# Kernel optimization log

Measured on AMD Instinct MI355X. Metric: run time of the kernel, lower is better.

Reference implementation:

```python
import jax, jax.numpy as jnp
import numpy as np

WINDOW = 128
CAUSAL = True
LOOK_BACKWARD = 1
LOOK_FORWARD = 0  # causal forces look_forward = 0


def _look_around(x, backward, forward, pad_value, dim):
    # pad along window axis (axis=1), then concat shifted slices along `dim`
    nw = x.shape[1]
    pad_cfg = [(0, 0)] * x.ndim
    pad_cfg[1] = (backward, forward)
    padded = jnp.pad(x, pad_cfg, constant_values=pad_value)
    slices = [padded[:, i:i + nw] for i in range(forward + backward + 1)]
    return jnp.concatenate(slices, axis=dim)


def setup_inputs() -> dict:
    key = jax.random.key(0)
    kq, kk, kv = jax.random.split(key, 3)
    shape = (2, 16, 4096, 64)
    return {
        "q": jax.random.normal(kq, shape, dtype=jnp.float32),
        "k": jax.random.normal(kk, shape, dtype=jnp.float32),
        "v": jax.random.normal(kv, shape, dtype=jnp.float32),
    }


def reference(q, k, v):
    b, h, t, e = q.shape
    scale = e ** (-0.5)
    windows = t // WINDOW  # t assumed divisible by WINDOW (pad_to_multiple is no-op)

    # merge batch and heads, bucket into windows
    bq = q.reshape(b * h, windows, WINDOW, e)
    bk = k.reshape(b * h, windows, WINDOW, e)
    bv = v.reshape(b * h, windows, WINDOW, e)

    # look-around gather of key/value windows: j-dim = WINDOW*(1+back+fwd)
    bk = _look_around(bk, LOOK_BACKWARD, LOOK_FORWARD, 0.0, dim=2)
    bv = _look_around(bv, LOOK_BACKWARD, LOOK_FORWARD, 0.0, dim=2)

    # positional indices for masking
    bq_t = jnp.arange(t).reshape(1, windows, WINDOW)
    bq_k = _look_around(bq_t, LOOK_BACKWARD, LOOK_FORWARD, -1, dim=2)

    mask = (bq_k == -1)[:, :, None, :]  # (1, w, 1, j) padded positions
    if CAUSAL:
        mask = mask | (bq_t[:, :, :, None] < bq_k[:, :, None, :])

    dots = jnp.einsum('bwie,bwje->bwij', bq * scale, bk)
    mask_value = -jnp.finfo(dots.dtype).max
    dots = jnp.where(mask, mask_value, dots)
    attn = jax.nn.softmax(dots.astype(jnp.float32), axis=-1).astype(dots.dtype)
    out = jnp.einsum('bwij,bwje->bwie', attn, bv)
    return out.reshape(b, h, t, e)
```

## Files before the change

### kernel.cpp

```cpp
#include <hip/hip_runtime.h>

#define T_DIM 4096
#define E_DIM 64
#define WIN   128
#define NWIN  (T_DIM / WIN)
#define KS_LD 72
#define VT_LD 136
#define PS_LD 36

typedef __bf16  bf16x8 __attribute__((ext_vector_type(8)));
typedef __bf16  bf16x4 __attribute__((ext_vector_type(4)));
typedef float   f32x16 __attribute__((ext_vector_type(16)));

template<int CTRL>
__device__ __forceinline__ float dppf(float x) {
  return __int_as_float(__builtin_amdgcn_update_dpp(0, __float_as_int(x), CTRL, 0xf, 0xf, false));
}
__device__ __forceinline__ float rsum32(float x) {
  x += dppf<0xB1>(x);
  x += dppf<0x4E>(x);
  x += dppf<0x141>(x);
  x += dppf<0x140>(x);
  x += __int_as_float(__builtin_amdgcn_ds_swizzle(__float_as_int(x), 0x401F));
  return x;
}

__global__ __launch_bounds__(256, 3)
void la_fwd(const float* __restrict__ Q, const float* __restrict__ K,
            const float* __restrict__ V, float* __restrict__ O)
{
  __shared__ __bf16 Ks[WIN * KS_LD];
  __shared__ __bf16 Vt[E_DIM * VT_LD];
  __shared__ __bf16 Psm[4 * 32 * PS_LD];

  const int tid  = threadIdx.x;
  const int lane = tid & 63;
  const int wid  = tid >> 6;
  const int col  = lane & 31;
  const int half = lane >> 5;

  const int w  = blockIdx.x;
  const int bh = blockIdx.y;

  const float* Qb = Q + (size_t)bh * T_DIM * E_DIM;
  const float* Kb = K + (size_t)bh * T_DIM * E_DIM;
  const float* Vb = V + (size_t)bh * T_DIM * E_DIM;
  float*       Ob = O + (size_t)bh * T_DIM * E_DIM;

  const int q0 = w * WIN;

  const float QS = 0.125f * 1.44269504088896340736f;
  bf16x8 aq[4];
  {
    const float* qrow = Qb + (size_t)(q0 + wid * 32 + col) * E_DIM;
#pragma unroll
    for (int c = 0; c < 4; ++c) {
      const float* p = qrow + c * 16 + half * 8;
      const float4 x = *(const float4*)(p);
      const float4 y = *(const float4*)(p + 4);
      bf16x8 a;
      a[0]=(__bf16)(x.x*QS); a[1]=(__bf16)(x.y*QS); a[2]=(__bf16)(x.z*QS); a[3]=(__bf16)(x.w*QS);
      a[4]=(__bf16)(y.x*QS); a[5]=(__bf16)(y.y*QS); a[6]=(__bf16)(y.z*QS); a[7]=(__bf16)(y.w*QS);
      aq[c] = a;
    }
  }

  float lr[16];
  f32x16 oacc[2];
#pragma unroll
  for (int r = 0; r < 16; ++r) lr[r] = 0.0f;
#pragma unroll
  for (int et = 0; et < 2; ++et)
#pragma unroll
    for (int r = 0; r < 16; ++r) oacc[et][r] = 0.0f;

  __bf16* Ps = Psm + wid * (32 * PS_LD);

  auto stage = [&](int kr0) {
    const float* kp = Kb + (size_t)kr0 * E_DIM;
#pragma unroll 4
    for (int i = 0; i < 8; ++i) {
      const int fi = (i << 10) + (tid << 2);
      const float4 kv = *(const float4*)(kp + fi);
      const int row = fi >> 6, cole = fi & 63;
      bf16x4 k4; k4[0]=(__bf16)kv.x; k4[1]=(__bf16)kv.y; k4[2]=(__bf16)kv.z; k4[3]=(__bf16)kv.w;
      *(bf16x4*)(&Ks[row * KS_LD + cole]) = k4;
    }
    const int j  = tid & 127;
    const int ch = (tid >> 7) * 32;
    const float* vrow = Vb + (size_t)(kr0 + j) * E_DIM + ch;
#pragma unroll 4
    for (int c4 = 0; c4 < 8; ++c4) {
      const float4 vv = *(const float4*)(vrow + c4 * 4);
      const int e = ch + c4 * 4;
      Vt[(e + 0) * VT_LD + j] = (__bf16)vv.x;
      Vt[(e + 1) * VT_LD + j] = (__bf16)vv.y;
      Vt[(e + 2) * VT_LD + j] = (__bf16)vv.z;
      Vt[(e + 3) * VT_LD + j] = (__bf16)vv.w;
    }
  };

  auto kb_step = [&](int kb, bool diag) {
    f32x16 s;
#pragma unroll
    for (int r = 0; r < 16; ++r) s[r] = 0.0f;
#pragma unroll
    for (int c = 0; c < 4; ++c) {
      const bf16x8 bk = *(const bf16x8*)(&Ks[(kb * 32 + col) * KS_LD + c * 16 + half * 8]);
      s = __builtin_amdgcn_mfma_f32_32x32x16_bf16(aq[c], bk, s, 0, 0, 0);
    }
#pragma unroll
    for (int r = 0; r < 16; ++r) {
      const int row = (r & 3) + 8 * (r >> 2) + 4 * half;
      float sv = s[r];
      if (diag && col > row) sv = -3.0e38f;
      const float p = __builtin_amdgcn_exp2f(sv);
      lr[r] += p;
      Ps[row * PS_LD + col] = (__bf16)p;
    }
    bf16x8 ap[2];
#pragma unroll
    for (int c2 = 0; c2 < 2; ++c2) {
      const __bf16* rp = Ps + col * PS_LD + c2 * 16 + half * 8;
      union { bf16x8 v8; bf16x4 v4[2]; } u;
      u.v4[0] = *(const bf16x4*)(rp);
      u.v4[1] = *(const bf16x4*)(rp + 4);
      ap[c2] = u.v8;
    }
#pragma unroll
    for (int c2 = 0; c2 < 2; ++c2) {
      const int j0 = kb * 32 + c2 * 16 + half * 8;
#pragma unroll
      for (int et = 0; et < 2; ++et) {
        const bf16x8 bv = *(const bf16x8*)(&Vt[(et * 32 + col) * VT_LD + j0]);
        oacc[et] = __builtin_amdgcn_mfma_f32_32x32x16_bf16(ap[c2], bv, oacc[et], 0, 0, 0);
      }
    }
  };

  if (w > 0) {
    stage(q0 - WIN);
    __syncthreads();
#pragma unroll
    for (int kb = 0; kb < 4; ++kb) kb_step(kb, false);
    __syncthreads();
  }

  stage(q0);
  __syncthreads();
  for (int kb = 0; kb <= wid; ++kb) kb_step(kb, kb == wid);

#pragma unroll
  for (int r = 0; r < 16; ++r) {
    const int row  = (r & 3) + 8 * (r >> 2) + 4 * half;
    const float rinv = __builtin_amdgcn_rcpf(rsum32(lr[r]));
    float* op = Ob + (size_t)(q0 + wid * 32 + row) * E_DIM;
    op[col]      = oacc[0][r] * rinv;
    op[col + 32] = oacc[1][r] * rinv;
  }
}

extern "C" void kernel_launch(void* const* d_in, const int* in_sizes, int n_in,
                              void* d_out, int out_size, void* d_ws, size_t ws_size,
                              hipStream_t stream) {
  const float* Q = (const float*)d_in[0];
  const float* K = (const float*)d_in[1];
  const float* V = (const float*)d_in[2];
  float*       O = (float*)d_out;
  const int bh = in_sizes[0] / (T_DIM * E_DIM);
  dim3 grid(NWIN, bh);
  la_fwd<<<grid, 256, 0, stream>>>(Q, K, V, O);
}
```

Measured before the change: 148.3 us.

## Compute transposed S so P stays in registers; read K directly from global

```diff
diff --git a/kernel.cpp b/kernel.cpp
--- a/kernel.cpp
+++ b/kernel.cpp
@@ -4,34 +4,17 @@
 #define E_DIM 64
 #define WIN   128
 #define NWIN  (T_DIM / WIN)
-#define KS_LD 72
 #define VT_LD 136
-#define PS_LD 36
 
 typedef __bf16  bf16x8 __attribute__((ext_vector_type(8)));
-typedef __bf16  bf16x4 __attribute__((ext_vector_type(4)));
 typedef float   f32x16 __attribute__((ext_vector_type(16)));
 
-template<int CTRL>
-__device__ __forceinline__ float dppf(float x) {
-  return __int_as_float(__builtin_amdgcn_update_dpp(0, __float_as_int(x), CTRL, 0xf, 0xf, false));
-}
-__device__ __forceinline__ float rsum32(float x) {
-  x += dppf<0xB1>(x);
-  x += dppf<0x4E>(x);
-  x += dppf<0x141>(x);
-  x += dppf<0x140>(x);
-  x += __int_as_float(__builtin_amdgcn_ds_swizzle(__float_as_int(x), 0x401F));
-  return x;
-}
-
-__global__ __launch_bounds__(256, 3)
+__global__ __launch_bounds__(256, 4)
 void la_fwd(const float* __restrict__ Q, const float* __restrict__ K,
             const float* __restrict__ V, float* __restrict__ O)
 {
-  __shared__ __bf16 Ks[WIN * KS_LD];
-  __shared__ __bf16 Vt[E_DIM * VT_LD];
-  __shared__ __bf16 Psm[4 * 32 * PS_LD];
+  __shared__ __align__(16) __bf16 Vt0[E_DIM * VT_LD];
+  __shared__ __align__(16) __bf16 Vt1[E_DIM * VT_LD];
 
   const int tid  = threadIdx.x;
   const int lane = tid & 63;
@@ -49,8 +32,25 @@
 
   const int q0 = w * WIN;
 
+  auto stage = [&](int kr0, __bf16* Vt) {
+    const int j  = tid & 127;
+    const int ch = (tid >> 7) * 32;
+    const float* vrow = Vb + (size_t)(kr0 + j) * E_DIM + ch;
+#pragma unroll
+    for (int c4 = 0; c4 < 8; ++c4) {
+      const float4 vv = *(const float4*)(vrow + c4 * 4);
+      const int e = ch + c4 * 4;
+      Vt[(e + 0) * VT_LD + j] = (__bf16)vv.x;
+      Vt[(e + 1) * VT_LD + j] = (__bf16)vv.y;
+      Vt[(e + 2) * VT_LD + j] = (__bf16)vv.z;
+      Vt[(e + 3) * VT_LD + j] = (__bf16)vv.w;
+    }
+  };
+  if (w > 0) stage(q0 - WIN, Vt0);
+  stage(q0, Vt1);
+
   const float QS = 0.125f * 1.44269504088896340736f;
-  bf16x8 aq[4];
+  bf16x8 bq[4];
   {
     const float* qrow = Qb + (size_t)(q0 + wid * 32 + col) * E_DIM;
 #pragma unroll
@@ -61,99 +61,85 @@
       bf16x8 a;
       a[0]=(__bf16)(x.x*QS); a[1]=(__bf16)(x.y*QS); a[2]=(__bf16)(x.z*QS); a[3]=(__bf16)(x.w*QS);
       a[4]=(__bf16)(y.x*QS); a[5]=(__bf16)(y.y*QS); a[6]=(__bf16)(y.z*QS); a[7]=(__bf16)(y.w*QS);
-      aq[c] = a;
+      bq[c] = a;
     }
   }
 
-  float lr[16];
+  float  lsum = 0.0f;
   f32x16 oacc[2];
-#pragma unroll
-  for (int r = 0; r < 16; ++r) lr[r] = 0.0f;
 #pragma unroll
   for (int et = 0; et < 2; ++et)
 #pragma unroll
     for (int r = 0; r < 16; ++r) oacc[et][r] = 0.0f;
 
-  __bf16* Ps = Psm + wid * (32 * PS_LD);
+  __syncthreads();
 
-  auto stage = [&](int kr0) {
-    const float* kp = Kb + (size_t)kr0 * E_DIM;
-#pragma unroll 4
-    for (int i = 0; i < 8; ++i) {
-      const int fi = (i << 10) + (tid << 2);
-      const float4 kv = *(const float4*)(kp + fi);
-      const int row = fi >> 6, cole = fi & 63;
-      bf16x4 k4; k4[0]=(__bf16)kv.x; k4[1]=(__bf16)kv.y; k4[2]=(__bf16)kv.z; k4[3]=(__bf16)kv.w;
-      *(bf16x4*)(&Ks[row * KS_LD + cole]) = k4;
-    }
-    const int j  = tid & 127;
-    const int ch = (tid >> 7) * 32;
-    const float* vrow = Vb + (size_t)(kr0 + j) * E_DIM + ch;
-#pragma unroll 4
-    for (int c4 = 0; c4 < 8; ++c4) {
-      const float4 vv = *(const float4*)(vrow + c4 * 4);
-      const int e = ch + c4 * 4;
-      Vt[(e + 0) * VT_LD + j] = (__bf16)vv.x;
-      Vt[(e + 1) * VT_LD + j] = (__bf16)vv.y;
-      Vt[(e + 2) * VT_LD + j] = (__bf16)vv.z;
-      Vt[(e + 3) * VT_LD + j] = (__bf16)vv.w;
-    }
-  };
-
-  auto kb_step = [&](int kb, bool diag) {
+  auto kb_step = [&](const float* krows, const __bf16* Vt, int kbj0, bool diag) {
     f32x16 s;
 #pragma unroll
     for (int r = 0; r < 16; ++r) s[r] = 0.0f;
 #pragma unroll
     for (int c = 0; c < 4; ++c) {
-      const bf16x8 bk = *(const bf16x8*)(&Ks[(kb * 32 + col) * KS_LD + c * 16 + half * 8]);
-      s = __builtin_amdgcn_mfma_f32_32x32x16_bf16(aq[c], bk, s, 0, 0, 0);
+      const float* p = krows + (size_t)col * E_DIM + c * 16 + half * 8;
+      const float4 x = *(const float4*)(p);
+      const float4 y = *(const float4*)(p + 4);
+      bf16x8 a;
+      a[0]=(__bf16)x.x; a[1]=(__bf16)x.y; a[2]=(__bf16)x.z; a[3]=(__bf16)x.w;
+      a[4]=(__bf16)y.x; a[5]=(__bf16)y.y; a[6]=(__bf16)y.z; a[7]=(__bf16)y.w;
+      s = __builtin_amdgcn_mfma_f32_32x32x16_bf16(a, bq[c], s, 0, 0, 0);
+    }
+    float pr[16];
+#pragma unroll
+    for (int r = 0; r < 16; ++r) {
+      const int key = (r & 3) + 8 * (r >> 2) + 4 * half;
+      float sv = s[r];
+      if (diag && key > col) sv = -3.0e38f;
+      const float p = __builtin_amdgcn_exp2f(sv);
+      lsum += p;
+      pr[r] = p;
     }
 #pragma unroll
-    for (int r = 0; r < 16; ++r) {
-      const int row = (r & 3) + 8 * (r >> 2) + 4 * half;
-      float sv = s[r];
-      if (diag && col > row) sv = -3.0e38f;
-      const float p = __builtin_amdgcn_exp2f(sv);
-      lr[r] += p;
-      Ps[row * PS_LD + col] = (__bf16)p;
-    }
-    bf16x8 ap[2];
-#pragma unroll
-    for (int c2 = 0; c2 < 2; ++c2) {
-      const __bf16* rp = Ps + col * PS_LD + c2 * 16 + half * 8;
-      union { bf16x8 v8; bf16x4 v4[2]; } u;
-      u.v4[0] = *(const bf16x4*)(rp);
-      u.v4[1] = *(const bf16x4*)(rp + 4);
-      ap[c2] = u.v8;
-    }
-#pragma unroll
-    for (int c2 = 0; c2 < 2; ++c2) {
-      const int j0 = kb * 32 + c2 * 16 + half * 8;
+    for (int g = 0; g < 2; ++g) {
+      int A0, A1, B0, B1;
+      asm("v_cvt_pk_bf16_f32 %0, %1, %2" : "=v"(A0) : "v"(pr[8*g+0]), "v"(pr[8*g+1]));
+      asm("v_cvt_pk_bf16_f32 %0, %1, %2" : "=v"(A1) : "v"(pr[8*g+2]), "v"(pr[8*g+3]));
+      asm("v_cvt_pk_bf16_f32 %0, %1, %2" : "=v"(B0) : "v"(pr[8*g+4]), "v"(pr[8*g+5]));
+      asm("v_cvt_pk_bf16_f32 %0, %1, %2" : "=v"(B1) : "v"(pr[8*g+6]), "v"(pr[8*g+7]));
+      asm("v_permlane32_swap_b32 %0, %1" : "+v"(A0), "+v"(B0));
+      asm("v_permlane32_swap_b32 %0, %1" : "+v"(A1), "+v"(B1));
+      union { int d[4]; bf16x8 v; } u;
+      u.d[0] = A0; u.d[1] = A1; u.d[2] = B0; u.d[3] = B1;
+      const int j0 = kbj0 + g * 16 + half * 8;
 #pragma unroll
       for (int et = 0; et < 2; ++et) {
         const bf16x8 bv = *(const bf16x8*)(&Vt[(et * 32 + col) * VT_LD + j0]);
-        oacc[et] = __builtin_amdgcn_mfma_f32_32x32x16_bf16(ap[c2], bv, oacc[et], 0, 0, 0);
+        oacc[et] = __builtin_amdgcn_mfma_f32_32x32x16_bf16(u.v, bv, oacc[et], 0, 0, 0);
       }
     }
   };
 
   if (w > 0) {
-    stage(q0 - WIN);
-    __syncthreads();
+    const float* kp = Kb + (size_t)(q0 - WIN) * E_DIM;
 #pragma unroll
-    for (int kb = 0; kb < 4; ++kb) kb_step(kb, false);
-    __syncthreads();
+    for (int kb = 0; kb < 4; ++kb)
+      kb_step(kp + (size_t)kb * 32 * E_DIM, Vt0, kb * 32, false);
   }
 
-  stage(q0);
-  __syncthreads();
-  for (int kb = 0; kb <= wid; ++kb) kb_step(kb, kb == wid);
+  {
+    const float* kp = Kb + (size_t)q0 * E_DIM;
+#pragma unroll
+    for (int kb = 0; kb < 4; ++kb)
+      if (kb <= wid) kb_step(kp + (size_t)kb * 32 * E_DIM, Vt1, kb * 32, kb == wid);
+  }
 
+  float xx = lsum, yy = lsum;
+  asm("v_permlane32_swap_b32 %0, %1" : "+v"(xx), "+v"(yy));
+  const float ltot = xx + yy;
 #pragma unroll
   for (int r = 0; r < 16; ++r) {
-    const int row  = (r & 3) + 8 * (r >> 2) + 4 * half;
-    const float rinv = __builtin_amdgcn_rcpf(rsum32(lr[r]));
+    const int row = (r & 3) + 8 * (r >> 2) + 4 * half;
+    const float lq   = __int_as_float(__builtin_amdgcn_ds_bpermute(row << 2, __float_as_int(ltot)));
+    const float rinv = __builtin_amdgcn_rcpf(lq);
     float* op = Ob + (size_t)(q0 + wid * 32 + row) * E_DIM;
     op[col]      = oacc[0][r] * rinv;
     op[col + 32] = oacc[1][r] * rinv;
```

After: 152.9 us. 3.1% more time.
